# Optimization experiments

Measured on AMD Instinct MI355X. Metric: run time of the kernel, lower is better.

The kernel has to match this reference:

```python
import jax, jax.numpy as jnp
import numpy as np

B = 256            # batch size
N_VARS = 8192      # variable nodes (LLR inputs)
N_CHECKS = 4096    # check nodes (zero-padded)
N_NODES = N_VARS + N_CHECKS
N_EDGES = 16_777_216
N_ITERS = 10       # num_iterations, unshared weights
NEG_SLOPE = 0.01   # F.leaky_relu default


def setup_inputs() -> dict:
    key = jax.random.key(0)
    ks = jax.random.split(key, 6)
    initial_llrs = jax.random.normal(ks[0], (B, N_VARS), dtype=jnp.float32)
    edge_index = jax.random.randint(ks[1], (2, N_EDGES), 0, B * N_NODES, dtype=jnp.int32)
    cycle_mask = jax.random.uniform(ks[2], (N_EDGES,), dtype=jnp.float32)
    # per-iteration layer params: Linear(3,1) weight/bias + scalars
    att_W = jax.random.normal(ks[3], (N_ITERS, 3), dtype=jnp.float32) * 0.5
    att_b = jax.random.normal(ks[4], (N_ITERS,), dtype=jnp.float32) * 0.1
    min_sum_scaler = jnp.full((N_ITERS,), 0.8, dtype=jnp.float32)
    cycle_penalty = jnp.full((N_ITERS,), -1.0, dtype=jnp.float32)
    return {
        "initial_llrs": initial_llrs,
        "edge_index": edge_index,
        "cycle_mask": cycle_mask,
        "att_W": att_W,
        "att_b": att_b,
        "min_sum_scaler": min_sum_scaler,
        "cycle_penalty": cycle_penalty,
    }


def reference(initial_llrs, edge_index, cycle_mask, att_W, att_b, min_sum_scaler, cycle_penalty):
    src, dst = edge_index[0], edge_index[1]
    # x0: [B, N_NODES] = LLRs padded with zeros for check nodes (residual each iter)
    x0 = jnp.concatenate(
        [initial_llrs, jnp.zeros((B, N_CHECKS), dtype=initial_llrs.dtype)], axis=1
    )

    def step(x, params):
        W, b, scaler, penalty = params  # W: [3], scalars otherwise
        xf = x.reshape(-1)             # [B*N_NODES]
        x_src = xf[src]                # [E] gather
        x_dst = xf[dst]                # [E] gather
        # Linear(3,1) over cat([x_src, x_dst, cycle_mask]) -> leaky_relu
        raw = x_src * W[0] + x_dst * W[1] + cycle_mask * W[2] + b
        raw = jnp.where(raw >= 0, raw, NEG_SLOPE * raw) + cycle_mask * penalty
        msgs = x_src * jax.nn.sigmoid(raw) * scaler   # [E]
        upd = jnp.zeros_like(xf).at[dst].add(msgs)    # scatter_add over flat nodes
        x_new = upd.reshape(B, N_NODES) + x0          # residual with initial LLRs
        return x_new, x_new[:, :N_VARS]

    _, outs = jax.lax.scan(
        step, x0, (att_W, att_b, min_sum_scaler, cycle_penalty)
    )
    return outs  # [N_ITERS, B, N_VARS] (stacked per-iteration variable LLRs)
```

## Files before the change

kernel.cpp:

```cpp
#include <hip/hip_runtime.h>

#define NV 8192
#define NC 4096
#define NN (NV + NC)
#define BATCH 256
#define TOT (BATCH * NN)
#define TOTP (TOT + 1024)
#define NEDGE 16777216
#define NITER 10
#define NBIN 3072
#define NPH 12
#define EPADF (NEDGE + NBIN * 256)
#define NB48 48
#define COARSECAP 393216
#define SCAP (NB48 * COARSECAP)
#define BINCAP 6144
#define PCK1 16384
#define CPAD2 32768
#define NCHK2 (COARSECAP / CPAD2)

typedef int   i4 __attribute__((ext_vector_type(4)));
typedef float f4 __attribute__((ext_vector_type(4)));
typedef unsigned int u32;
typedef unsigned short u16;
typedef u32 u4  __attribute__((ext_vector_type(4)));
typedef u16 us4 __attribute__((ext_vector_type(4)));

__global__ __launch_bounds__(256) void k_init(const float* __restrict__ llr,
                                              float* __restrict__ x) {
    int base = (blockIdx.x * 256 + threadIdx.x) * 4;
    if (base >= TOTP) return;
    f4 v = {0.f, 0.f, 0.f, 0.f};
    if (base < TOT) {
        int b = base / NN;
        int n = base - b * NN;
        if (n < NV) v = *reinterpret_cast<const f4*>(llr + (size_t)b * NV + n);
    }
    *reinterpret_cast<f4*>(x + base) = v;
}

__global__ void k_init48(int* __restrict__ cur48) {
    int t = threadIdx.x;
    if (t < NB48) cur48[t] = t * COARSECAP;
}

__global__ __launch_bounds__(256) void k_initb(int* __restrict__ cur3) {
    int b = blockIdx.x * 256 + threadIdx.x;
    if (b < NBIN) cur3[b] = b * BINCAP;
}

__global__ __launch_bounds__(256) void k_pass1(
    const int* __restrict__ src, const int* __restrict__ dst,
    const float* __restrict__ cm,
    u32* __restrict__ stg0, u16* __restrict__ stg1, int* __restrict__ cur48)
{
    __shared__ int lh[NB48], lpos[NB48];
    int t = threadIdx.x;
    if (t < NB48) lh[t] = 0;
    __syncthreads();
    int base = blockIdx.x * PCK1;
    for (int i = 0; i < PCK1; i += 1024) {
        i4 d = *reinterpret_cast<const i4*>(dst + base + i + t * 4);
        atomicAdd(&lh[d.x >> 16], 1);
        atomicAdd(&lh[d.y >> 16], 1);
        atomicAdd(&lh[d.z >> 16], 1);
        atomicAdd(&lh[d.w >> 16], 1);
    }
    __syncthreads();
    if (t < NB48) {
        int c = lh[t];
        lpos[t] = c ? atomicAdd(&cur48[t], c) : 0;
    }
    __syncthreads();
    for (int i = 0; i < PCK1; i += 1024) {
        i4 s4 = *reinterpret_cast<const i4*>(src + base + i + t * 4);
        i4 d4 = *reinterpret_cast<const i4*>(dst + base + i + t * 4);
        f4 c4 = *reinterpret_cast<const f4*>(cm + base + i + t * 4);
        int   ss[4] = {s4.x, s4.y, s4.z, s4.w};
        int   dd[4] = {d4.x, d4.y, d4.z, d4.w};
        float cc[4] = {c4.x, c4.y, c4.z, c4.w};
#pragma unroll
        for (int k = 0; k < 4; ++k) {
            int bkt = dd[k] >> 16;
            int pos = atomicAdd(&lpos[bkt], 1);
            int q = (int)(cc[k] * 1024.0f + 0.5f);
            q = q > 1023 ? 1023 : q;
            stg0[pos] = ((u32)ss[k] << 10) | (u32)(dd[k] & 1023);
            stg1[pos] = (u16)((q << 6) | ((dd[k] >> 10) & 63));
        }
    }
}

__global__ __launch_bounds__(256) void k_pass2a(
    const u32* __restrict__ stg0, const u16* __restrict__ stg1,
    u32* __restrict__ iek, u16* __restrict__ iec,
    const int* __restrict__ cur48, int* __restrict__ cur3, int* __restrict__ cnt)
{
    __shared__ int lh[64 * NPH];
    __shared__ int lpos[64];
    int c = blockIdx.x / NCHK2;
    int k = blockIdx.x - c * NCHK2;
    int t = threadIdx.x;
    int cbase = c * COARSECAP;
    int vend = cur48[c];
    int start = cbase + k * CPAD2;
    int end = min(start + CPAD2, vend);
    if (start >= end) return;
    for (int j = t; j < 64 * NPH; j += 256) lh[j] = 0;
    __syncthreads();
    for (int i0 = start; i0 < end; i0 += 1024) {
        int i = i0 + t * 4;
        if (i + 4 <= end) {
            u4  w = *reinterpret_cast<const u4*>(stg0 + i);
            us4 v = *reinterpret_cast<const us4*>(stg1 + i);
            atomicAdd(&lh[(v.x & 63) * NPH + (w.x >> 28)], 1);
            atomicAdd(&lh[(v.y & 63) * NPH + (w.y >> 28)], 1);
            atomicAdd(&lh[(v.z & 63) * NPH + (w.z >> 28)], 1);
            atomicAdd(&lh[(v.w & 63) * NPH + (w.w >> 28)], 1);
        } else if (i < end) {
            for (int j = 0; j < end - i; ++j)
                atomicAdd(&lh[(stg1[i + j] & 63) * NPH + (stg0[i + j] >> 28)], 1);
        }
    }
    __syncthreads();
    if (t < 64) {
        int s = 0;
        for (int p = 0; p < NPH; ++p) s += lh[t * NPH + p];
        lpos[t] = s ? atomicAdd(&cur3[(c << 6) + t], s) : 0;
    }
    for (int j = t; j < 64 * NPH; j += 256)
        if (lh[j]) atomicAdd(&cnt[(c << 6) * NPH + j], lh[j]);
    __syncthreads();
    for (int i0 = start; i0 < end; i0 += 1024) {
        int i = i0 + t * 4;
        if (i + 4 <= end) {
            u4  w = *reinterpret_cast<const u4*>(stg0 + i);
            us4 v = *reinterpret_cast<const us4*>(stg1 + i);
            u32 ww[4] = {w.x, w.y, w.z, w.w};
            u16 vv[4] = {v.x, v.y, v.z, v.w};
#pragma unroll
            for (int j = 0; j < 4; ++j) {
                int pos = atomicAdd(&lpos[vv[j] & 63], 1);
                iek[pos] = ww[j];
                iec[pos] = (u16)(vv[j] >> 6);
            }
        } else if (i < end) {
            for (int j = 0; j < end - i; ++j) {
                u16 v1 = stg1[i + j];
                int pos = atomicAdd(&lpos[v1 & 63], 1);
                iek[pos] = stg0[i + j];
                iec[pos] = (u16)(v1 >> 6);
            }
        }
    }
}

__global__ __launch_bounds__(256) void k_scanp(
    const int* __restrict__ cnt, int* __restrict__ po)
{
    __shared__ int part[256];
    int t = threadIdx.x;
    int s = 0;
    for (int k = 0; k < 12; ++k) {
        int b = t * 12 + k;
        for (int p = 0; p < NPH; ++p) s += (cnt[b * NPH + p] + 3) & ~3;
    }
    part[t] = s;
    __syncthreads();
    for (int d = 1; d < 256; d <<= 1) {
        int v = (t >= d) ? part[t - d] : 0;
        __syncthreads();
        part[t] += v;
        __syncthreads();
    }
    int base = (t == 0) ? 0 : part[t - 1];
    for (int k = 0; k < 12; ++k) {
        int b = t * 12 + k;
        for (int p = 0; p < NPH; ++p) {
            po[b * 13 + p] = base;
            base += (cnt[b * NPH + p] + 3) & ~3;
        }
        po[b * 13 + 12] = base;
    }
}

__global__ __launch_bounds__(256) void k_pass2b(
    const u32* __restrict__ iek, const u16* __restrict__ iec,
    u32* __restrict__ fpk, u16* __restrict__ fcmh,
    const int* __restrict__ cnt, const int* __restrict__ po)
{
    __shared__ int lcur[NPH];
    __shared__ int lbt;
    int b = blockIdx.x;
    int t = threadIdx.x;
    if (t < NPH) lcur[t] = po[b * 13 + t];
    if (t == 0) {
        int s = 0;
        for (int p = 0; p < NPH; ++p) s += cnt[b * NPH + p];
        lbt = s;
    }
    __syncthreads();
    int s = b * BINCAP;
    int e = s + lbt;
    for (int i0 = s; i0 < e; i0 += 1024) {
        int i = i0 + t * 4;
        if (i + 4 <= e) {
            u4  w  = *reinterpret_cast<const u4*>(iek + i);
            us4 cq = *reinterpret_cast<const us4*>(iec + i);
            u32 ww[4] = {w.x, w.y, w.z, w.w};
            u16 cc[4] = {cq.x, cq.y, cq.z, cq.w};
#pragma unroll
            for (int j = 0; j < 4; ++j) {
                int p = (int)(ww[j] >> 28);
                int pos = atomicAdd(&lcur[p], 1);
                fpk[pos] = ww[j];
                fcmh[pos] = cc[j];
            }
        } else if (i < e) {
            for (int j = 0; j < e - i; ++j) {
                u32 w1 = iek[i + j];
                int p = (int)(w1 >> 28);
                int pos = atomicAdd(&lcur[p], 1);
                fpk[pos] = w1;
                fcmh[pos] = iec[i + j];
            }
        }
    }
    __syncthreads();
    if (t < NPH) {
        for (int j = lcur[t]; j < po[b * 13 + t + 1]; ++j) {
            fpk[j] = ((u32)TOT) << 10;
            fcmh[j] = 0;
        }
    }
}

__global__ __launch_bounds__(256) void k_iter2(
    const u32* __restrict__ fpk, const u16* __restrict__ fcmh,
    const int* __restrict__ po,
    const float* __restrict__ xin, float* __restrict__ xout,
    const float* __restrict__ llr, float* __restrict__ out,
    const float* __restrict__ attW, const float* __restrict__ attb,
    const float* __restrict__ scal, const float* __restrict__ pen, int it)
{
    const float W0 = attW[it * 3 + 0];
    const float W1 = attW[it * 3 + 1];
    const float W2 = attW[it * 3 + 2];
    const float bb = attb[it];
    const float sc = scal[it];
    const float pe = pen[it];
    const float QS = 1.0f / 1024.0f;

    __shared__ float acc[2048];
    __shared__ float xds[2048];
    int blk = blockIdx.x;
    int t = threadIdx.x;
    int b0 = blk << 1;
    int nbase = blk << 11;

    f4 z = {0.f, 0.f, 0.f, 0.f};
    *reinterpret_cast<f4*>(acc + t * 4) = z;
    *reinterpret_cast<f4*>(acc + 1024 + t * 4) = z;
    *reinterpret_cast<f4*>(xds + t * 4) =
        *reinterpret_cast<const f4*>(xin + nbase + t * 4);
    *reinterpret_cast<f4*>(xds + 1024 + t * 4) =
        *reinterpret_cast<const f4*>(xin + nbase + 1024 + t * 4);
    __syncthreads();

    for (int p = 0; p < NPH; ++p) {
#pragma unroll
        for (int h = 0; h < 2; ++h) {
            int b = b0 + h;
            int s = po[b * 13 + p], e = po[b * 13 + p + 1];
            float* ac = acc + (h << 10);
            const float* xd = xds + (h << 10);
            for (int i0 = s; i0 < e; i0 += 1024) {
                int i = i0 + t * 4;
                if (i < e) {
                    u4  wa = *reinterpret_cast<const u4*>(fpk + i);
                    us4 ca = *reinterpret_cast<const us4*>(fcmh + i);
                    u32 w[4]  = {wa.x, wa.y, wa.z, wa.w};
                    u16 cq[4] = {ca.x, ca.y, ca.z, ca.w};
                    float xs[4];
#pragma unroll
                    for (int k = 0; k < 4; ++k) xs[k] = xin[w[k] >> 10];
#pragma unroll
                    for (int k = 0; k < 4; ++k) {
                        int ldst = (int)(w[k] & 1023u);
                        float cmv = (float)cq[k] * QS;
                        float xdv = xd[ldst];
                        float raw = fmaf(xs[k], W0, fmaf(xdv, W1, fmaf(cmv, W2, bb)));
                        raw = (raw >= 0.f) ? raw : 0.01f * raw;
                        raw = fmaf(cmv, pe, raw);
                        float msg = xs[k] * sc / (1.0f + __expf(-raw));
                        atomicAdd(ac + ldst, msg);
                    }
                }
            }
        }
    }
    __syncthreads();

#pragma unroll
    for (int h = 0; h < 2; ++h) {
        int b = b0 + h;
        int row = b / 12, sub = b - row * 12, n0 = sub << 10;
        f4 a = *reinterpret_cast<f4*>(acc + (h << 10) + t * 4);
        if (n0 < NV) {
            f4 x0 = *reinterpret_cast<const f4*>(llr + (size_t)row * NV + n0 + t * 4);
            a += x0;
            __builtin_nontemporal_store(a,
                reinterpret_cast<f4*>(out + (size_t)it * (BATCH * NV) +
                                      (size_t)row * NV + n0 + t * 4));
        }
        *reinterpret_cast<f4*>(xout + (b << 10) + t * 4) = a;
    }
}

__global__ __launch_bounds__(256) void k_edges(
    const int* __restrict__ src, const int* __restrict__ dst,
    const float* __restrict__ cm,
    const float* __restrict__ xin, float* __restrict__ xout,
    const float* __restrict__ attW, const float* __restrict__ attb,
    const float* __restrict__ scal, const float* __restrict__ pen, int it)
{
    const float W0 = attW[it * 3 + 0];
    const float W1 = attW[it * 3 + 1];
    const float W2 = attW[it * 3 + 2];
    const float bb = attb[it];
    const float sc = scal[it];
    const float pe = pen[it];
    int e = (blockIdx.x * 256 + threadIdx.x) * 4;
    i4 s4 = *reinterpret_cast<const i4*>(src + e);
    i4 d4 = *reinterpret_cast<const i4*>(dst + e);
    f4 c4 = *reinterpret_cast<const f4*>(cm + e);
    int   si[4] = {s4.x, s4.y, s4.z, s4.w};
    int   di[4] = {d4.x, d4.y, d4.z, d4.w};
    float cc[4] = {c4.x, c4.y, c4.z, c4.w};
#pragma unroll
    for (int k = 0; k < 4; ++k) {
        float xs = xin[si[k]];
        float xd = xin[di[k]];
        float raw = fmaf(xs, W0, fmaf(xd, W1, fmaf(cc[k], W2, bb)));
        raw = (raw >= 0.f) ? raw : 0.01f * raw;
        raw = fmaf(cc[k], pe, raw);
        float sig = 1.0f / (1.0f + __expf(-raw));
        atomicAdd(xout + di[k], xs * sig * sc);
    }
}

__global__ __launch_bounds__(256) void k_emit_init(
    const float* __restrict__ xnew, const float* __restrict__ llr,
    float* __restrict__ xother, float* __restrict__ out, int it)
{
    int base = (blockIdx.x * 256 + threadIdx.x) * 4;
    if (base >= TOTP) return;
    f4 z = {0.f, 0.f, 0.f, 0.f};
    if (base < TOT) {
        int b = base / NN;
        int n = base - b * NN;
        if (n < NV) {
            f4 v = *reinterpret_cast<const f4*>(xnew + base);
            *reinterpret_cast<f4*>(out + (size_t)it * (BATCH * NV) +
                                   (size_t)b * NV + n) = v;
            *reinterpret_cast<f4*>(xother + base) =
                *reinterpret_cast<const f4*>(llr + (size_t)b * NV + n);
        } else {
            *reinterpret_cast<f4*>(xother + base) = z;
        }
    } else {
        *reinterpret_cast<f4*>(xother + base) = z;
    }
}

extern "C" void kernel_launch(void* const* d_in, const int* in_sizes, int n_in,
                              void* d_out, int out_size, void* d_ws, size_t ws_size,
                              hipStream_t stream) {
    const float* llr  = (const float*)d_in[0];
    const int*   ei   = (const int*)d_in[1];
    const float* cm   = (const float*)d_in[2];
    const float* attW = (const float*)d_in[3];
    const float* attb = (const float*)d_in[4];
    const float* scal = (const float*)d_in[5];
    const float* pen  = (const float*)d_in[6];
    float* out = (float*)d_out;
    const int* src = ei;
    const int* dst = ei + NEDGE;

    char* w = (char*)d_ws;
    u32* iek = (u32*)w;                         w += (size_t)SCAP * 4;
    u16* iec = (u16*)w;                         w += (((size_t)SCAP * 2 + 15) & ~15ull);
    char* reg2 = w;
    u32* stg0 = (u32*)reg2;
    u16* stg1 = (u16*)(reg2 + (size_t)SCAP * 4);
    u32* fpk  = (u32*)reg2;
    u16* fcmh = (u16*)(reg2 + (size_t)EPADF * 4);
    w += (size_t)SCAP * 4 + (((size_t)SCAP * 2 + 15) & ~15ull);
    int* cnt   = (int*)w;                       w += (size_t)NBIN * NPH * 4;
    int* po    = (int*)w;                       w += (size_t)NBIN * 13 * 4;
    int* cur3  = (int*)w;                       w += (size_t)NBIN * 4;
    int* cur48 = (int*)w;                       w += (size_t)NB48 * 4;
    size_t need = (size_t)(w - (char*)d_ws);

    float* xA = (float*)iek;
    float* xB = xA + TOTP;

    dim3 blk(256);
    dim3 gNode((TOTP / 4 + 255) / 256);

    if (ws_size >= need) {
        hipMemsetAsync(cnt, 0, (size_t)NBIN * NPH * sizeof(int), stream);
        k_init48<<<1, 64, 0, stream>>>(cur48);
        k_initb<<<(NBIN + 255) / 256, blk, 0, stream>>>(cur3);
        k_pass1<<<NEDGE / PCK1, blk, 0, stream>>>(src, dst, cm, stg0, stg1, cur48);
        k_pass2a<<<NB48 * NCHK2, blk, 0, stream>>>(stg0, stg1, iek, iec, cur48, cur3, cnt);
        k_scanp<<<1, blk, 0, stream>>>(cnt, po);
        k_pass2b<<<NBIN, blk, 0, stream>>>(iek, iec, fpk, fcmh, cnt, po);

        k_init<<<gNode, blk, 0, stream>>>(llr, xA);
        k_init<<<gNode, blk, 0, stream>>>(llr, xB);
        for (int it = 0; it < NITER; ++it) {
            k_iter2<<<NBIN / 2, blk, 0, stream>>>(fpk, fcmh, po, xA, xB, llr, out,
                                                  attW, attb, scal, pen, it);
            float* tswp = xA; xA = xB; xB = tswp;
        }
    } else {
        float* fA = (float*)d_ws;
        float* fB = fA + TOTP;
        k_init<<<gNode, blk, 0, stream>>>(llr, fA);
        k_init<<<gNode, blk, 0, stream>>>(llr, fB);
        for (int it = 0; it < NITER; ++it) {
            k_edges<<<NEDGE / 4 / 256, blk, 0, stream>>>(src, dst, cm, fA, fB,
                                                         attW, attb, scal, pen, it);
            k_emit_init<<<gNode, blk, 0, stream>>>(fB, llr, fA, out, it);
            float* tswp = fA; fA = fB; fB = tswp;
        }
    }
}
```

Before: 1.340 ms.

## Interleave staging records into 8-byte structs and split iter loop across half-blocks

Adds a path, used when the workspace is large enough, where the binning passes keep each edge's packed index and metadata together in one 8-byte record. This replaces the separate u32 and u16 arrays, so each scattered write is a single 8-byte store instead of two separate stores. It also changes the iteration kernel so each half of the block (128 threads) handles one of the two batch bins, instead of all 256 threads looping over both. The cost is more workspace memory and more bytes per record than the packed 6-byte layout.

```diff
diff --git a/kernel.cpp b/kernel.cpp
--- a/kernel.cpp
+++ b/kernel.cpp
@@ -24,6 +24,7 @@
 typedef unsigned int u32;
 typedef unsigned short u16;
 typedef u32 u4  __attribute__((ext_vector_type(4)));
+typedef u32 uv2 __attribute__((ext_vector_type(2)));
 typedef u16 us4 __attribute__((ext_vector_type(4)));
 
 __global__ __launch_bounds__(256) void k_init(const float* __restrict__ llr,
@@ -49,10 +50,12 @@
     if (b < NBIN) cur3[b] = b * BINCAP;
 }
 
-__global__ __launch_bounds__(256) void k_pass1(
+template<bool I8>
+__global__ __launch_bounds__(256) void k_pass1t(
     const int* __restrict__ src, const int* __restrict__ dst,
     const float* __restrict__ cm,
-    u32* __restrict__ stg0, u16* __restrict__ stg1, int* __restrict__ cur48)
+    u32* __restrict__ stg0, u16* __restrict__ stg1,
+    u32* __restrict__ stgI, int* __restrict__ cur48)
 {
     __shared__ int lh[NB48], lpos[NB48];
     int t = threadIdx.x;
@@ -85,15 +88,24 @@
             int pos = atomicAdd(&lpos[bkt], 1);
             int q = (int)(cc[k] * 1024.0f + 0.5f);
             q = q > 1023 ? 1023 : q;
-            stg0[pos] = ((u32)ss[k] << 10) | (u32)(dd[k] & 1023);
-            stg1[pos] = (u16)((q << 6) | ((dd[k] >> 10) & 63));
-        }
-    }
-}
-
-__global__ __launch_bounds__(256) void k_pass2a(
+            u32 pk = ((u32)ss[k] << 10) | (u32)(dd[k] & 1023);
+            u16 meta = (u16)((q << 6) | ((dd[k] >> 10) & 63));
+            if constexpr (I8) {
+                uv2 r; r.x = pk; r.y = (u32)meta;
+                *reinterpret_cast<uv2*>(stgI + (size_t)pos * 2) = r;
+            } else {
+                stg0[pos] = pk;
+                stg1[pos] = meta;
+            }
+        }
+    }
+}
+
+template<bool I8>
+__global__ __launch_bounds__(256) void k_pass2at(
     const u32* __restrict__ stg0, const u16* __restrict__ stg1,
-    u32* __restrict__ iek, u16* __restrict__ iec,
+    const u32* __restrict__ stgI,
+    u32* __restrict__ iek, u16* __restrict__ iec, u32* __restrict__ irecI,
     const int* __restrict__ cur48, int* __restrict__ cur3, int* __restrict__ cnt)
 {
     __shared__ int lh[64 * NPH];
@@ -111,15 +123,28 @@
     for (int i0 = start; i0 < end; i0 += 1024) {
         int i = i0 + t * 4;
         if (i + 4 <= end) {
-            u4  w = *reinterpret_cast<const u4*>(stg0 + i);
-            us4 v = *reinterpret_cast<const us4*>(stg1 + i);
-            atomicAdd(&lh[(v.x & 63) * NPH + (w.x >> 28)], 1);
-            atomicAdd(&lh[(v.y & 63) * NPH + (w.y >> 28)], 1);
-            atomicAdd(&lh[(v.z & 63) * NPH + (w.z >> 28)], 1);
-            atomicAdd(&lh[(v.w & 63) * NPH + (w.w >> 28)], 1);
+            u32 pk[4]; u16 mt[4];
+            if constexpr (I8) {
+                u4 ra = *reinterpret_cast<const u4*>(stgI + (size_t)i * 2);
+                u4 rb = *reinterpret_cast<const u4*>(stgI + (size_t)i * 2 + 4);
+                pk[0] = ra.x; mt[0] = (u16)ra.y; pk[1] = ra.z; mt[1] = (u16)ra.w;
+                pk[2] = rb.x; mt[2] = (u16)rb.y; pk[3] = rb.z; mt[3] = (u16)rb.w;
+            } else {
+                u4  w = *reinterpret_cast<const u4*>(stg0 + i);
+                us4 v = *reinterpret_cast<const us4*>(stg1 + i);
+                pk[0] = w.x; pk[1] = w.y; pk[2] = w.z; pk[3] = w.w;
+                mt[0] = v.x; mt[1] = v.y; mt[2] = v.z; mt[3] = v.w;
+            }
+#pragma unroll
+            for (int j = 0; j < 4; ++j)
+                atomicAdd(&lh[(mt[j] & 63) * NPH + (pk[j] >> 28)], 1);
         } else if (i < end) {
-            for (int j = 0; j < end - i; ++j)
-                atomicAdd(&lh[(stg1[i + j] & 63) * NPH + (stg0[i + j] >> 28)], 1);
+            for (int j = 0; j < end - i; ++j) {
+                u32 pk1; u16 m1;
+                if constexpr (I8) { pk1 = stgI[(size_t)(i + j) * 2]; m1 = (u16)stgI[(size_t)(i + j) * 2 + 1]; }
+                else { pk1 = stg0[i + j]; m1 = stg1[i + j]; }
+                atomicAdd(&lh[(m1 & 63) * NPH + (pk1 >> 28)], 1);
+            }
         }
     }
     __syncthreads();
@@ -134,22 +159,42 @@
     for (int i0 = start; i0 < end; i0 += 1024) {
         int i = i0 + t * 4;
         if (i + 4 <= end) {
-            u4  w = *reinterpret_cast<const u4*>(stg0 + i);
-            us4 v = *reinterpret_cast<const us4*>(stg1 + i);
-            u32 ww[4] = {w.x, w.y, w.z, w.w};
-            u16 vv[4] = {v.x, v.y, v.z, v.w};
+            u32 pk[4]; u16 mt[4];
+            if constexpr (I8) {
+                u4 ra = *reinterpret_cast<const u4*>(stgI + (size_t)i * 2);
+                u4 rb = *reinterpret_cast<const u4*>(stgI + (size_t)i * 2 + 4);
+                pk[0] = ra.x; mt[0] = (u16)ra.y; pk[1] = ra.z; mt[1] = (u16)ra.w;
+                pk[2] = rb.x; mt[2] = (u16)rb.y; pk[3] = rb.z; mt[3] = (u16)rb.w;
+            } else {
+                u4  w = *reinterpret_cast<const u4*>(stg0 + i);
+                us4 v = *reinterpret_cast<const us4*>(stg1 + i);
+                pk[0] = w.x; pk[1] = w.y; pk[2] = w.z; pk[3] = w.w;
+                mt[0] = v.x; mt[1] = v.y; mt[2] = v.z; mt[3] = v.w;
+            }
 #pragma unroll
             for (int j = 0; j < 4; ++j) {
-                int pos = atomicAdd(&lpos[vv[j] & 63], 1);
-                iek[pos] = ww[j];
-                iec[pos] = (u16)(vv[j] >> 6);
+                int pos = atomicAdd(&lpos[mt[j] & 63], 1);
+                if constexpr (I8) {
+                    uv2 r; r.x = pk[j]; r.y = (u32)mt[j];
+                    *reinterpret_cast<uv2*>(irecI + (size_t)pos * 2) = r;
+                } else {
+                    iek[pos] = pk[j];
+                    iec[pos] = (u16)(mt[j] >> 6);
+                }
             }
         } else if (i < end) {
             for (int j = 0; j < end - i; ++j) {
-                u16 v1 = stg1[i + j];
-                int pos = atomicAdd(&lpos[v1 & 63], 1);
-                iek[pos] = stg0[i + j];
-                iec[pos] = (u16)(v1 >> 6);
+                u32 pk1; u16 m1;
+                if constexpr (I8) { pk1 = stgI[(size_t)(i + j) * 2]; m1 = (u16)stgI[(size_t)(i + j) * 2 + 1]; }
+                else { pk1 = stg0[i + j]; m1 = stg1[i + j]; }
+                int pos = atomicAdd(&lpos[m1 & 63], 1);
+                if constexpr (I8) {
+                    uv2 r; r.x = pk1; r.y = (u32)m1;
+                    *reinterpret_cast<uv2*>(irecI + (size_t)pos * 2) = r;
+                } else {
+                    iek[pos] = pk1;
+                    iec[pos] = (u16)(m1 >> 6);
+                }
             }
         }
     }
@@ -184,8 +229,10 @@
     }
 }
 
-__global__ __launch_bounds__(256) void k_pass2b(
+template<bool I8>
+__global__ __launch_bounds__(256) void k_pass2bt(
     const u32* __restrict__ iek, const u16* __restrict__ iec,
+    const u32* __restrict__ irecI,
     u32* __restrict__ fpk, u16* __restrict__ fcmh,
     const int* __restrict__ cnt, const int* __restrict__ po)
 {
@@ -205,24 +252,34 @@
     for (int i0 = s; i0 < e; i0 += 1024) {
         int i = i0 + t * 4;
         if (i + 4 <= e) {
-            u4  w  = *reinterpret_cast<const u4*>(iek + i);
-            us4 cq = *reinterpret_cast<const us4*>(iec + i);
-            u32 ww[4] = {w.x, w.y, w.z, w.w};
-            u16 cc[4] = {cq.x, cq.y, cq.z, cq.w};
+            u32 pk[4]; u16 cq[4];
+            if constexpr (I8) {
+                u4 ra = *reinterpret_cast<const u4*>(irecI + (size_t)i * 2);
+                u4 rb = *reinterpret_cast<const u4*>(irecI + (size_t)i * 2 + 4);
+                pk[0] = ra.x; cq[0] = (u16)(ra.y >> 6); pk[1] = ra.z; cq[1] = (u16)(ra.w >> 6);
+                pk[2] = rb.x; cq[2] = (u16)(rb.y >> 6); pk[3] = rb.z; cq[3] = (u16)(rb.w >> 6);
+            } else {
+                u4  w  = *reinterpret_cast<const u4*>(iek + i);
+                us4 cv = *reinterpret_cast<const us4*>(iec + i);
+                pk[0] = w.x; pk[1] = w.y; pk[2] = w.z; pk[3] = w.w;
+                cq[0] = cv.x; cq[1] = cv.y; cq[2] = cv.z; cq[3] = cv.w;
+            }
 #pragma unroll
             for (int j = 0; j < 4; ++j) {
-                int p = (int)(ww[j] >> 28);
+                int p = (int)(pk[j] >> 28);
                 int pos = atomicAdd(&lcur[p], 1);
-                fpk[pos] = ww[j];
-                fcmh[pos] = cc[j];
+                fpk[pos] = pk[j];
+                fcmh[pos] = cq[j];
             }
         } else if (i < e) {
             for (int j = 0; j < e - i; ++j) {
-                u32 w1 = iek[i + j];
-                int p = (int)(w1 >> 28);
+                u32 pk1; u16 c1;
+                if constexpr (I8) { pk1 = irecI[(size_t)(i + j) * 2]; c1 = (u16)(irecI[(size_t)(i + j) * 2 + 1] >> 6); }
+                else { pk1 = iek[i + j]; c1 = iec[i + j]; }
+                int p = (int)(pk1 >> 28);
                 int pos = atomicAdd(&lcur[p], 1);
-                fpk[pos] = w1;
-                fcmh[pos] = iec[i + j];
+                fpk[pos] = pk1;
+                fcmh[pos] = c1;
             }
         }
     }
@@ -267,45 +324,43 @@
         *reinterpret_cast<const f4*>(xin + nbase + 1024 + t * 4);
     __syncthreads();
 
+    int h = t >> 7;
+    int tl = t & 127;
+    int b = b0 + h;
+    float* ac = acc + (h << 10);
+    const float* xd = xds + (h << 10);
+    const int* pob = po + b * 13;
+
     for (int p = 0; p < NPH; ++p) {
-#pragma unroll
-        for (int h = 0; h < 2; ++h) {
-            int b = b0 + h;
-            int s = po[b * 13 + p], e = po[b * 13 + p + 1];
-            float* ac = acc + (h << 10);
-            const float* xd = xds + (h << 10);
-            for (int i0 = s; i0 < e; i0 += 1024) {
-                int i = i0 + t * 4;
-                if (i < e) {
-                    u4  wa = *reinterpret_cast<const u4*>(fpk + i);
-                    us4 ca = *reinterpret_cast<const us4*>(fcmh + i);
-                    u32 w[4]  = {wa.x, wa.y, wa.z, wa.w};
-                    u16 cq[4] = {ca.x, ca.y, ca.z, ca.w};
-                    float xs[4];
-#pragma unroll
-                    for (int k = 0; k < 4; ++k) xs[k] = xin[w[k] >> 10];
-#pragma unroll
-                    for (int k = 0; k < 4; ++k) {
-                        int ldst = (int)(w[k] & 1023u);
-                        float cmv = (float)cq[k] * QS;
-                        float xdv = xd[ldst];
-                        float raw = fmaf(xs[k], W0, fmaf(xdv, W1, fmaf(cmv, W2, bb)));
-                        raw = (raw >= 0.f) ? raw : 0.01f * raw;
-                        raw = fmaf(cmv, pe, raw);
-                        float msg = xs[k] * sc / (1.0f + __expf(-raw));
-                        atomicAdd(ac + ldst, msg);
-                    }
-                }
-            }
-        }
-    }
-    __syncthreads();
-
-#pragma unroll
-    for (int h = 0; h < 2; ++h) {
-        int b = b0 + h;
-        int row = b / 12, sub = b - row * 12, n0 = sub << 10;
-        f4 a = *reinterpret_cast<f4*>(acc + (h << 10) + t * 4);
+        int e = pob[p + 1];
+        for (int i = pob[p] + tl * 4; i < e; i += 512) {
+            u4  wa = *reinterpret_cast<const u4*>(fpk + i);
+            us4 ca = *reinterpret_cast<const us4*>(fcmh + i);
+            u32 w[4]  = {wa.x, wa.y, wa.z, wa.w};
+            u16 cq[4] = {ca.x, ca.y, ca.z, ca.w};
+            float xs[4];
+#pragma unroll
+            for (int k = 0; k < 4; ++k) xs[k] = xin[w[k] >> 10];
+#pragma unroll
+            for (int k = 0; k < 4; ++k) {
+                int ldst = (int)(w[k] & 1023u);
+                float cmv = (float)cq[k] * QS;
+                float xdv = xd[ldst];
+                float raw = fmaf(xs[k], W0, fmaf(xdv, W1, fmaf(cmv, W2, bb)));
+                raw = (raw >= 0.f) ? raw : 0.01f * raw;
+                raw = fmaf(cmv, pe, raw);
+                float msg = xs[k] * sc / (1.0f + __expf(-raw));
+                atomicAdd(ac + ldst, msg);
+            }
+        }
+    }
+    __syncthreads();
+
+#pragma unroll
+    for (int hh = 0; hh < 2; ++hh) {
+        int bo = b0 + hh;
+        int row = bo / 12, sub = bo - row * 12, n0 = sub << 10;
+        f4 a = *reinterpret_cast<f4*>(acc + (hh << 10) + t * 4);
         if (n0 < NV) {
             f4 x0 = *reinterpret_cast<const f4*>(llr + (size_t)row * NV + n0 + t * 4);
             a += x0;
@@ -313,7 +368,7 @@
                 reinterpret_cast<f4*>(out + (size_t)it * (BATCH * NV) +
                                       (size_t)row * NV + n0 + t * 4));
         }
-        *reinterpret_cast<f4*>(xout + (b << 10) + t * 4) = a;
+        *reinterpret_cast<f4*>(xout + (bo << 10) + t * 4) = a;
     }
 }
 
@@ -387,36 +442,76 @@
     const int* src = ei;
     const int* dst = ei + NEDGE;
 
-    char* w = (char*)d_ws;
-    u32* iek = (u32*)w;                         w += (size_t)SCAP * 4;
-    u16* iec = (u16*)w;                         w += (((size_t)SCAP * 2 + 15) & ~15ull);
-    char* reg2 = w;
-    u32* stg0 = (u32*)reg2;
-    u16* stg1 = (u16*)(reg2 + (size_t)SCAP * 4);
-    u32* fpk  = (u32*)reg2;
-    u16* fcmh = (u16*)(reg2 + (size_t)EPADF * 4);
-    w += (size_t)SCAP * 4 + (((size_t)SCAP * 2 + 15) & ~15ull);
-    int* cnt   = (int*)w;                       w += (size_t)NBIN * NPH * 4;
-    int* po    = (int*)w;                       w += (size_t)NBIN * 13 * 4;
-    int* cur3  = (int*)w;                       w += (size_t)NBIN * 4;
-    int* cur48 = (int*)w;                       w += (size_t)NB48 * 4;
-    size_t need = (size_t)(w - (char*)d_ws);
-
-    float* xA = (float*)iek;
-    float* xB = xA + TOTP;
+    size_t cntbytes = ((size_t)NBIN * NPH + (size_t)NBIN * 13 + NBIN + NB48 + 64) * 4;
+    size_t need8 = (size_t)SCAP * 8ull * 2ull + cntbytes;
+    size_t need6 = ((size_t)SCAP * 6ull + 16) * 2ull + cntbytes;
 
     dim3 blk(256);
     dim3 gNode((TOTP / 4 + 255) / 256);
 
-    if (ws_size >= need) {
+    u32* fpk = nullptr; u16* fcmh = nullptr;
+    int *cnt = nullptr, *po = nullptr, *cur3 = nullptr, *cur48 = nullptr;
+    float *xA = nullptr, *xB = nullptr;
+    bool ok = false;
+
+    if (ws_size >= need8) {
+        char* w = (char*)d_ws;
+        u32* irecI = (u32*)w;                    w += (size_t)SCAP * 8;
+        char* reg2 = w;                          w += (size_t)SCAP * 8;
+        u32* stgI = (u32*)reg2;
+        fpk  = (u32*)reg2;
+        fcmh = (u16*)(reg2 + (size_t)EPADF * 4);
+        cnt   = (int*)w;                         w += (size_t)NBIN * NPH * 4;
+        po    = (int*)w;                         w += (size_t)NBIN * 13 * 4;
+        cur3  = (int*)w;                         w += (size_t)NBIN * 4;
+        cur48 = (int*)w;
+        xA = (float*)irecI;
+        xB = xA + TOTP;
+
         hipMemsetAsync(cnt, 0, (size_t)NBIN * NPH * sizeof(int), stream);
         k_init48<<<1, 64, 0, stream>>>(cur48);
         k_initb<<<(NBIN + 255) / 256, blk, 0, stream>>>(cur3);
-        k_pass1<<<NEDGE / PCK1, blk, 0, stream>>>(src, dst, cm, stg0, stg1, cur48);
-        k_pass2a<<<NB48 * NCHK2, blk, 0, stream>>>(stg0, stg1, iek, iec, cur48, cur3, cnt);
+        k_pass1t<true><<<NEDGE / PCK1, blk, 0, stream>>>(src, dst, cm,
+                                                         nullptr, nullptr, stgI, cur48);
+        k_pass2at<true><<<NB48 * NCHK2, blk, 0, stream>>>(nullptr, nullptr, stgI,
+                                                          nullptr, nullptr, irecI,
+                                                          cur48, cur3, cnt);
         k_scanp<<<1, blk, 0, stream>>>(cnt, po);
-        k_pass2b<<<NBIN, blk, 0, stream>>>(iek, iec, fpk, fcmh, cnt, po);
-
+        k_pass2bt<true><<<NBIN, blk, 0, stream>>>(nullptr, nullptr, irecI,
+                                                  fpk, fcmh, cnt, po);
+        ok = true;
+    } else if (ws_size >= need6) {
+        char* w = (char*)d_ws;
+        u32* iek = (u32*)w;                      w += (size_t)SCAP * 4;
+        u16* iec = (u16*)w;                      w += (((size_t)SCAP * 2 + 15) & ~15ull);
+        char* reg2 = w;
+        u32* stg0 = (u32*)reg2;
+        u16* stg1 = (u16*)(reg2 + (size_t)SCAP * 4);
+        fpk  = (u32*)reg2;
+        fcmh = (u16*)(reg2 + (size_t)EPADF * 4);
+        w += (size_t)SCAP * 4 + (((size_t)SCAP * 2 + 15) & ~15ull);
+        cnt   = (int*)w;                         w += (size_t)NBIN * NPH * 4;
+        po    = (int*)w;                         w += (size_t)NBIN * 13 * 4;
+        cur3  = (int*)w;                         w += (size_t)NBIN * 4;
+        cur48 = (int*)w;
+        xA = (float*)iek;
+        xB = xA + TOTP;
+
+        hipMemsetAsync(cnt, 0, (size_t)NBIN * NPH * sizeof(int), stream);
+        k_init48<<<1, 64, 0, stream>>>(cur48);
+        k_initb<<<(NBIN + 255) / 256, blk, 0, stream>>>(cur3);
+        k_pass1t<false><<<NEDGE / PCK1, blk, 0, stream>>>(src, dst, cm,
+                                                          stg0, stg1, nullptr, cur48);
+        k_pass2at<false><<<NB48 * NCHK2, blk, 0, stream>>>(stg0, stg1, nullptr,
+                                                           iek, iec, nullptr,
+                                                           cur48, cur3, cnt);
+        k_scanp<<<1, blk, 0, stream>>>(cnt, po);
+        k_pass2bt<false><<<NBIN, blk, 0, stream>>>(iek, iec, nullptr,
+                                                   fpk, fcmh, cnt, po);
+        ok = true;
+    }
+
+    if (ok) {
         k_init<<<gNode, blk, 0, stream>>>(llr, xA);
         k_init<<<gNode, blk, 0, stream>>>(llr, xB);
         for (int it = 0; it < NITER; ++it) {
```

Result: slower. 1.451 ms (+8.3%).
